# Performance work log

Measured on AMD Instinct MI355X. Metric: run time of the kernel, lower is better.

Reference implementation:

```python
import jax, jax.numpy as jnp
import numpy as np

WINDOW = 25  # causal sliding-window size for trend extraction


def setup_inputs() -> dict:
    key = jax.random.key(0)
    kx, kw1, kb1, kw2, kb2 = jax.random.split(key, 5)
    T = 720
    bound = 1.0 / np.sqrt(T)
    x = jax.random.normal(kx, (32, 512, T), dtype=jnp.float32)
    trend_w = jax.random.uniform(kw1, (T, T), jnp.float32, -bound, bound)
    trend_b = jax.random.uniform(kb1, (T,), jnp.float32, -bound, bound)
    seasonal_w = jax.random.uniform(kw2, (T, T), jnp.float32, -bound, bound)
    seasonal_b = jax.random.uniform(kb2, (T,), jnp.float32, -bound, bound)
    return {"x": x, "trend_w": trend_w, "trend_b": trend_b,
            "seasonal_w": seasonal_w, "seasonal_b": seasonal_b}


def _causal_window_mean(x, window):
    # x: [B, N, T]; trend[..., j] = mean(x[..., max(0, j-window+1):j+1])
    T = x.shape[-1]
    cs = jnp.cumsum(x, axis=-1)
    cs_shift = jnp.concatenate(
        [jnp.zeros(x.shape[:-1] + (window,), x.dtype), cs[..., :T - window]], axis=-1)
    counts = jnp.minimum(jnp.arange(T) + 1, window).astype(x.dtype)
    return (cs - cs_shift) / counts


def reference(x, trend_w, trend_b, seasonal_w, seasonal_b):
    trend = _causal_window_mean(x, WINDOW)
    seasonal = x - trend
    trend_out = jnp.einsum('bnt,ut->bnu', trend, trend_w) + trend_b
    seasonal_out = jnp.einsum('bnt,ut->bnu', seasonal, seasonal_w) + seasonal_b
    return trend_out + seasonal_out
```

## Files before the change

kernel.cpp:

```cpp
#include <hip/hip_runtime.h>
#include <hip/hip_bf16.h>


#define Tdim  720
#define KP    736
#define WROWS 768
#define NK    23
#define BM    64
#define APAD  744

using bf16x8 = __attribute__((ext_vector_type(8))) __bf16;
using f32x4  = __attribute__((ext_vector_type(4))) float;

__global__ void fold_w_kernel(const float* __restrict__ tw,
                              const float* __restrict__ tb,
                              const float* __restrict__ sw,
                              const float* __restrict__ sb,
                              __bf16* __restrict__ Wb,
                              float* __restrict__ beff) {
  int idx = blockIdx.x * 256 + threadIdx.x;
  if (idx >= WROWS * KP) return;
  int u = idx / KP;
  int i = idx - u * KP;
  float w = 0.0f;
  if (u < Tdim && i < Tdim) {
    const float* twr = tw + (size_t)u * Tdim;
    const float* swr = sw + (size_t)u * Tdim;
    int tend = (i + 25 < Tdim) ? (i + 25) : Tdim;
    float acc = 0.0f;
    if (i >= 24) {
      #pragma unroll 5
      for (int t = i; t < tend; ++t) acc += twr[t] - swr[t];
      acc *= 0.04f;
    } else {
      for (int t = i; t < tend; ++t) {
        float c = (t >= 24) ? 0.04f : 1.0f / (float)(t + 1);
        acc += (twr[t] - swr[t]) * c;
      }
    }
    w = swr[i] + acc;
  }
  Wb[idx] = (__bf16)w;
  if (i == 0 && u < Tdim) beff[u] = tb[u] + sb[u];
}

__global__ __launch_bounds__(512, 1)
void dlinear_gemm(const float* __restrict__ x,
                  const __bf16* __restrict__ Wb,
                  const float* __restrict__ beff,
                  float* __restrict__ out) {
  __shared__ __bf16 As[BM * APAD];

  const int tid  = threadIdx.x;
  const int lane = tid & 63;
  const int wid  = tid >> 6;
  const int lg = lane >> 4, lr = lane & 15;

  const int m0 = blockIdx.x * BM;
  const int u0 = wid * 96;

  #pragma unroll
  for (int c = 0; c < 12; ++c) {
    int idx = tid + 512 * c;
    if (idx < BM * 90) {
      int row  = idx / 90;
      int col8 = idx - row * 90;
      const float* p = x + (size_t)(m0 + row) * Tdim + col8 * 8;
      f32x4 a0 = ((const f32x4*)p)[0];
      f32x4 a1 = ((const f32x4*)p)[1];
      bf16x8 v;
      #pragma unroll
      for (int j = 0; j < 4; ++j) { v[j] = (__bf16)a0[j]; v[j + 4] = (__bf16)a1[j]; }
      *(bf16x8*)(&As[row * APAD + col8 * 8]) = v;
    }
  }
  {
    int r = tid >> 3;
    int c = 720 + (tid & 7) * 2;
    As[r * APAD + c]     = (__bf16)0.0f;
    As[r * APAD + c + 1] = (__bf16)0.0f;
  }
  __syncthreads();

  const __bf16* wp[6];
  #pragma unroll
  for (int ni = 0; ni < 6; ++ni)
    wp[ni] = Wb + (size_t)(u0 + ni * 16 + lr) * KP + lg * 8;

  int arofs[4];
  #pragma unroll
  for (int mi = 0; mi < 4; ++mi) arofs[mi] = (mi * 16 + lr) * APAD + lg * 8;

  f32x4 acc[4][6];
  #pragma unroll
  for (int mi = 0; mi < 4; ++mi)
    #pragma unroll
    for (int ni = 0; ni < 6; ++ni) {
      f32x4 z; z[0] = 0.f; z[1] = 0.f; z[2] = 0.f; z[3] = 0.f;
      acc[mi][ni] = z;
    }

  bf16x8 b0[6], b1[6];
  #pragma unroll
  for (int ni = 0; ni < 6; ++ni) b0[ni] = *(const bf16x8*)wp[ni];

  for (int t = 0; t < NK - 1; t += 2) {
    #pragma unroll
    for (int ni = 0; ni < 6; ++ni) b1[ni] = *(const bf16x8*)(wp[ni] + (t + 1) * 32);
    {
      bf16x8 av[4];
      #pragma unroll
      for (int mi = 0; mi < 4; ++mi) av[mi] = *(const bf16x8*)(&As[arofs[mi] + t * 32]);
      #pragma unroll
      for (int mi = 0; mi < 4; ++mi)
        #pragma unroll
        for (int ni = 0; ni < 6; ++ni)
          acc[mi][ni] = __builtin_amdgcn_mfma_f32_16x16x32_bf16(av[mi], b0[ni],
                                                                acc[mi][ni], 0, 0, 0);
    }
    #pragma unroll
    for (int ni = 0; ni < 6; ++ni) b0[ni] = *(const bf16x8*)(wp[ni] + (t + 2) * 32);
    {
      bf16x8 av[4];
      #pragma unroll
      for (int mi = 0; mi < 4; ++mi) av[mi] = *(const bf16x8*)(&As[arofs[mi] + (t + 1) * 32]);
      #pragma unroll
      for (int mi = 0; mi < 4; ++mi)
        #pragma unroll
        for (int ni = 0; ni < 6; ++ni)
          acc[mi][ni] = __builtin_amdgcn_mfma_f32_16x16x32_bf16(av[mi], b1[ni],
                                                                acc[mi][ni], 0, 0, 0);
    }
  }
  {
    bf16x8 av[4];
    #pragma unroll
    for (int mi = 0; mi < 4; ++mi) av[mi] = *(const bf16x8*)(&As[arofs[mi] + 22 * 32]);
    #pragma unroll
    for (int mi = 0; mi < 4; ++mi)
      #pragma unroll
      for (int ni = 0; ni < 6; ++ni)
        acc[mi][ni] = __builtin_amdgcn_mfma_f32_16x16x32_bf16(av[mi], b0[ni],
                                                              acc[mi][ni], 0, 0, 0);
  }

  #pragma unroll
  for (int ni = 0; ni < 6; ++ni) {
    const int u = u0 + ni * 16 + lr;
    if (u >= Tdim) continue;
    const float bias = beff[u];
    #pragma unroll
    for (int mi = 0; mi < 4; ++mi) {
      const int mb = m0 + mi * 16 + lg * 4;
      #pragma unroll
      for (int j = 0; j < 4; ++j)
        out[(size_t)(mb + j) * Tdim + u] = acc[mi][ni][j] + bias;
    }
  }
}

extern "C" void kernel_launch(void* const* d_in, const int* in_sizes, int n_in,
                              void* d_out, int out_size, void* d_ws, size_t ws_size,
                              hipStream_t stream) {
  const float* x  = (const float*)d_in[0];
  const float* tw = (const float*)d_in[1];
  const float* tb = (const float*)d_in[2];
  const float* sw = (const float*)d_in[3];
  const float* sb = (const float*)d_in[4];
  float* out = (float*)d_out;

  __bf16* Wb  = (__bf16*)d_ws;
  float* beff = (float*)((char*)d_ws + (size_t)WROWS * KP * sizeof(__bf16));

  const int fold_total = WROWS * KP;
  fold_w_kernel<<<dim3((fold_total + 255) / 256), dim3(256), 0, stream>>>(
      tw, tb, sw, sb, Wb, beff);

  const int M = in_sizes[0] / Tdim;
  dim3 grid(M / BM);
  dlinear_gemm<<<grid, dim3(512), 0, stream>>>(x, Wb, beff, out);
}
```

Before: 48.88 us.

## Halve GEMM row tile to 32 and drop B double-buffering for higher occupancy

Halves the M tile per block from 64 to 32 rows, doubling the grid to 512 blocks, and raises the launch-bounds minimum to 4 blocks per CU. Removes the manual double-buffered prefetch of weight fragments in favour of a simple per-step load, which cuts register pressure. The intent is more resident waves per CU to hide global and LDS latency. In exchange each block re-reads the full weight matrix for half as many rows, doubling total weight traffic, and each step has less MFMA work to cover its loads.

```diff
diff --git a/kernel.cpp b/kernel.cpp
--- a/kernel.cpp
+++ b/kernel.cpp
@@ -6,7 +6,7 @@
 #define KP    736
 #define WROWS 768
 #define NK    23
-#define BM    64
+#define BM    32
 #define APAD  744
 
 using bf16x8 = __attribute__((ext_vector_type(8))) __bf16;
@@ -44,7 +44,7 @@
   if (i == 0 && u < Tdim) beff[u] = tb[u] + sb[u];
 }
 
-__global__ __launch_bounds__(512, 1)
+__global__ __launch_bounds__(512, 4)
 void dlinear_gemm(const float* __restrict__ x,
                   const __bf16* __restrict__ Wb,
                   const float* __restrict__ beff,
@@ -60,7 +60,7 @@
   const int u0 = wid * 96;
 
   #pragma unroll
-  for (int c = 0; c < 12; ++c) {
+  for (int c = 0; c < 6; ++c) {
     int idx = tid + 512 * c;
     if (idx < BM * 90) {
       int row  = idx / 90;
@@ -75,10 +75,9 @@
     }
   }
   {
-    int r = tid >> 3;
-    int c = 720 + (tid & 7) * 2;
-    As[r * APAD + c]     = (__bf16)0.0f;
-    As[r * APAD + c + 1] = (__bf16)0.0f;
+    int r = tid >> 4;
+    int c = 720 + (tid & 15);
+    As[r * APAD + c] = (__bf16)0.0f;
   }
   __syncthreads();
 
@@ -87,60 +86,31 @@
   for (int ni = 0; ni < 6; ++ni)
     wp[ni] = Wb + (size_t)(u0 + ni * 16 + lr) * KP + lg * 8;
 
-  int arofs[4];
+  int arofs[2];
   #pragma unroll
-  for (int mi = 0; mi < 4; ++mi) arofs[mi] = (mi * 16 + lr) * APAD + lg * 8;
+  for (int mi = 0; mi < 2; ++mi) arofs[mi] = (mi * 16 + lr) * APAD + lg * 8;
 
-  f32x4 acc[4][6];
+  f32x4 acc[2][6];
   #pragma unroll
-  for (int mi = 0; mi < 4; ++mi)
+  for (int mi = 0; mi < 2; ++mi)
     #pragma unroll
     for (int ni = 0; ni < 6; ++ni) {
       f32x4 z; z[0] = 0.f; z[1] = 0.f; z[2] = 0.f; z[3] = 0.f;
       acc[mi][ni] = z;
     }
 
-  bf16x8 b0[6], b1[6];
-  #pragma unroll
-  for (int ni = 0; ni < 6; ++ni) b0[ni] = *(const bf16x8*)wp[ni];
-
-  for (int t = 0; t < NK - 1; t += 2) {
+  for (int t = 0; t < NK; ++t) {
+    bf16x8 bv[6];
     #pragma unroll
-    for (int ni = 0; ni < 6; ++ni) b1[ni] = *(const bf16x8*)(wp[ni] + (t + 1) * 32);
-    {
-      bf16x8 av[4];
-      #pragma unroll
-      for (int mi = 0; mi < 4; ++mi) av[mi] = *(const bf16x8*)(&As[arofs[mi] + t * 32]);
-      #pragma unroll
-      for (int mi = 0; mi < 4; ++mi)
-        #pragma unroll
-        for (int ni = 0; ni < 6; ++ni)
-          acc[mi][ni] = __builtin_amdgcn_mfma_f32_16x16x32_bf16(av[mi], b0[ni],
-                                                                acc[mi][ni], 0, 0, 0);
-    }
+    for (int ni = 0; ni < 6; ++ni) bv[ni] = *(const bf16x8*)(wp[ni] + t * 32);
+    bf16x8 av[2];
     #pragma unroll
-    for (int ni = 0; ni < 6; ++ni) b0[ni] = *(const bf16x8*)(wp[ni] + (t + 2) * 32);
-    {
-      bf16x8 av[4];
-      #pragma unroll
-      for (int mi = 0; mi < 4; ++mi) av[mi] = *(const bf16x8*)(&As[arofs[mi] + (t + 1) * 32]);
-      #pragma unroll
-      for (int mi = 0; mi < 4; ++mi)
-        #pragma unroll
-        for (int ni = 0; ni < 6; ++ni)
-          acc[mi][ni] = __builtin_amdgcn_mfma_f32_16x16x32_bf16(av[mi], b1[ni],
-                                                                acc[mi][ni], 0, 0, 0);
-    }
-  }
-  {
-    bf16x8 av[4];
+    for (int mi = 0; mi < 2; ++mi) av[mi] = *(const bf16x8*)(&As[arofs[mi] + t * 32]);
     #pragma unroll
-    for (int mi = 0; mi < 4; ++mi) av[mi] = *(const bf16x8*)(&As[arofs[mi] + 22 * 32]);
-    #pragma unroll
-    for (int mi = 0; mi < 4; ++mi)
+    for (int mi = 0; mi < 2; ++mi)
       #pragma unroll
       for (int ni = 0; ni < 6; ++ni)
-        acc[mi][ni] = __builtin_amdgcn_mfma_f32_16x16x32_bf16(av[mi], b0[ni],
+        acc[mi][ni] = __builtin_amdgcn_mfma_f32_16x16x32_bf16(av[mi], bv[ni],
                                                               acc[mi][ni], 0, 0, 0);
   }
 
@@ -150,7 +120,7 @@
     if (u >= Tdim) continue;
     const float bias = beff[u];
     #pragma unroll
-    for (int mi = 0; mi < 4; ++mi) {
+    for (int mi = 0; mi < 2; ++mi) {
       const int mb = m0 + mi * 16 + lg * 4;
       #pragma unroll
       for (int j = 0; j < 4; ++j)
```

After: 67.50 us. 38.1% more time.
